# Optimization experiments

Measured on AMD Instinct MI355X. Metric: run time of the kernel, lower is better.

Reference implementation:

```python
import jax, jax.numpy as jnp
import numpy as np

B, N, F_IN, F_OUT, H = 2, 4096, 256, 64, 4


def setup_inputs() -> dict:
    key = jax.random.key(0)
    k_adj, k_h, k_w, k_l, k_r = jax.random.split(key, 5)
    adj = jax.random.randint(k_adj, (B, N, N), 0, 2, dtype=jnp.int32)
    h = jax.random.normal(k_h, (B, N, F_IN), dtype=jnp.float32)
    # xavier-uniform-ish params
    lim_w = float(np.sqrt(6.0 / (F_IN + F_OUT)))
    W = jax.random.uniform(k_w, (F_IN, F_OUT), jnp.float32, -lim_w, lim_w)
    lim_a = float(np.sqrt(6.0 / (F_OUT + H)))
    Wl = jax.random.uniform(k_l, (H, F_OUT), jnp.float32, -lim_a, lim_a)  # attn_l.weight
    Wr = jax.random.uniform(k_r, (H, F_OUT), jnp.float32, -lim_a, lim_a)  # attn_r.weight
    b = jnp.zeros((F_OUT,), jnp.float32)
    return {"adj": adj, "h": h, "W": W, "Wl": Wl, "Wr": Wr, "b": b}


def reference(adj, h, W, Wl, Wr, b):
    # dropout layers are identity in eval mode
    x = jnp.einsum('bnf,fo->bno', h, W)                       # (B,N,F_OUT)
    el = jnp.einsum('bno,ho->bnh', x, Wl)                     # (B,N,H)
    er = jnp.einsum('bno,ho->bnh', x, Wr)                     # (B,N,H)
    attn = el[:, :, None, :] + er[:, None, :, :]              # (B,N,N,H)
    attn = jax.nn.leaky_relu(attn, negative_slope=0.2)
    attn = jnp.where(adj[..., None] == 0, -jnp.inf, attn)
    attn = jax.nn.softmax(attn, axis=2)                       # softmax over source nodes j
    out = jnp.einsum('bijh,bjf->bihf', attn, x)               # (B,N,H,F_OUT)
    out = out + b                                             # bias over feature dim
    out = jax.nn.elu(out)                                     # activation
    return out.reshape(B, N, H * F_OUT)                       # n_heads>1 concat; B>1 keeps batch
```

## Files before the change

kernel.cpp:

```cpp
#include <hip/hip_runtime.h>
#include <hip/hip_bf16.h>


#define NN 4096
#define NH 4

typedef __bf16 bf16x8 __attribute__((ext_vector_type(8)));
typedef unsigned short ushortx8 __attribute__((ext_vector_type(8)));
typedef float f32x4 __attribute__((ext_vector_type(4)));

__device__ __forceinline__ void gload_lds16(const void* g, void* lds) {
  __builtin_amdgcn_global_load_lds(
      (const __attribute__((address_space(1))) void*)g,
      (__attribute__((address_space(3))) void*)lds, 16, 0, 0);
}

__device__ __forceinline__ unsigned short f2bf(float x) {
  __hip_bfloat16 hb = __float2bfloat16(x);
  return __builtin_bit_cast(unsigned short, hb);
}

__global__ __launch_bounds__(256) void gat_prep(
    const float* __restrict__ hmat, const float* __restrict__ W,
    const float* __restrict__ Wl, const float* __restrict__ Wr,
    unsigned short* __restrict__ xT, float* __restrict__ elT,
    float* __restrict__ erT)
{
  const int t = threadIdx.x;
  const int wv = t >> 6;
  const int l  = t & 63;
  const int b  = blockIdx.x >> 6;
  const int i0 = (blockIdx.x & 63) << 6;
  const int r0 = i0 + wv * 16;

  float wl[NH], wr[NH];
#pragma unroll
  for (int hh = 0; hh < NH; ++hh) { wl[hh] = Wl[hh*64 + l]; wr[hh] = Wr[hh*64 + l]; }

  float acc[16];
#pragma unroll
  for (int rr = 0; rr < 16; ++rr) acc[rr] = 0.f;

  const float* hbase = hmat + ((size_t)(b*NN + r0)) * 256;
  for (int k4 = 0; k4 < 64; ++k4) {
    float wv4[4];
#pragma unroll
    for (int kk = 0; kk < 4; ++kk) wv4[kk] = W[(k4*4 + kk)*64 + l];
#pragma unroll
    for (int rr = 0; rr < 16; ++rr) {
      const float4 hv = *(const float4*)(hbase + rr*256 + k4*4);
      acc[rr] = fmaf(hv.x, wv4[0], acc[rr]);
      acc[rr] = fmaf(hv.y, wv4[1], acc[rr]);
      acc[rr] = fmaf(hv.z, wv4[2], acc[rr]);
      acc[rr] = fmaf(hv.w, wv4[3], acc[rr]);
    }
  }

#pragma unroll
  for (int rr = 0; rr < 16; ++rr) {
    const int r = r0 + rr;
    xT[((size_t)(b*64 + l))*NN + r] = f2bf(acc[rr]);
#pragma unroll
    for (int hh = 0; hh < NH; ++hh) {
      float ev = acc[rr] * wl[hh];
      float rv = acc[rr] * wr[hh];
#pragma unroll
      for (int s = 1; s < 64; s <<= 1) {
        ev += __shfl_xor(ev, s, 64);
        rv += __shfl_xor(rv, s, 64);
      }
      if (l == 0) {
        elT[((size_t)b*NH + hh)*NN + r] = ev;
        erT[((size_t)b*NH + hh)*NN + r] = rv;
      }
    }
  }
}

__global__ __launch_bounds__(512, 2) void gat_main(
    const int* __restrict__ adj, const unsigned short* __restrict__ xT,
    const float* __restrict__ elT, const float* __restrict__ erT,
    const float* __restrict__ bias, float* __restrict__ out)
{
  __shared__ __align__(16) int            adj_lds[2][32*64];
  __shared__ __align__(16) unsigned short xt_lds[2][64*64];
  __shared__ __align__(16) float          er_lds[2][NH*64];
  __shared__ __align__(16) float          denom_lds[NH][32];

  const int t = threadIdx.x;
  const int w = t >> 6;
  const int l = t & 63;
  const int h = w >> 1;
  const int ihalf = w & 1;
  const int b  = blockIdx.x >> 7;
  const int i0 = (blockIdx.x & 127) << 5;

  const int lrow = l & 15;
  const int lk   = l >> 4;
  const int i_sc = (ihalf << 4) + lrow;
  const int swzi = (i_sc & 7) << 2;

  const float el_reg = elT[((size_t)b*NH + h)*NN + i0 + i_sc];

  auto issue_tile = [&](int j0, int bufi) {
    {
      const int ir = (w << 2) + (l >> 4);
      const int c  = (l & 15) ^ (ir & 7);
      gload_lds16(adj + ((size_t)(b*NN + i0 + ir))*NN + j0 + (c << 2),
                  &adj_lds[bufi][w*256]);
    }
    {
      const int fr_sub = l >> 3;
      const int c  = (l & 7) ^ fr_sub;
      gload_lds16(xT + ((size_t)(b*64 + (w<<3) + fr_sub))*NN + j0 + (c << 3),
                  &xt_lds[bufi][w*512]);
    }
    if (w == 0) {
      gload_lds16(erT + ((size_t)b*NH + (l >> 4))*NN + j0 + ((l & 15) << 2),
                  &er_lds[bufi][0]);
    }
  };

  f32x4 acc[4] = {};
  float dsum_acc = 0.f;

  issue_tile(0, 0);

  for (int it = 0; it < NN/64; ++it) {
    const int cur = it & 1;
    asm volatile("s_waitcnt vmcnt(0)" ::: "memory");
    __builtin_amdgcn_s_barrier();
    if (it + 1 < NN/64) issue_tile((it + 1) * 64, cur ^ 1);

    ushortx8 pa[2];
#pragma unroll
    for (int kc = 0; kc < 2; ++kc) {
      const int cbase = kc*32 + (lk << 3);
      const int4   aj0 = *(const int4*)  &adj_lds[cur][(i_sc*64 + cbase)     ^ swzi];
      const int4   aj1 = *(const int4*)  &adj_lds[cur][(i_sc*64 + cbase + 4) ^ swzi];
      const float4 er0 = *(const float4*)&er_lds[cur][h*64 + cbase];
      const float4 er1 = *(const float4*)&er_lds[cur][h*64 + cbase + 4];
#define SCORE(A, E, IDX) { \
        float s_ = el_reg + (E); \
        float lr_ = fmaxf(s_, 0.2f * s_); \
        float w_ = (A) ? __expf(lr_) : 0.0f; \
        dsum_acc += w_; \
        pa[kc][IDX] = f2bf(w_); }
      SCORE(aj0.x, er0.x, 0) SCORE(aj0.y, er0.y, 1)
      SCORE(aj0.z, er0.z, 2) SCORE(aj0.w, er0.w, 3)
      SCORE(aj1.x, er1.x, 4) SCORE(aj1.y, er1.y, 5)
      SCORE(aj1.z, er1.z, 6) SCORE(aj1.w, er1.w, 7)
#undef SCORE
    }

#pragma unroll
    for (int kc = 0; kc < 2; ++kc) {
      const bf16x8 A = __builtin_bit_cast(bf16x8, pa[kc]);
      const int jc = kc*32 + (lk << 3);
#pragma unroll
      for (int fq = 0; fq < 4; ++fq) {
        const int f = (fq << 4) + lrow;
        const int idx = (f*64 + jc) ^ ((f & 7) << 3);
        const bf16x8 B = __builtin_bit_cast(bf16x8, *(const ushortx8*)&xt_lds[cur][idx]);
        acc[fq] = __builtin_amdgcn_mfma_f32_16x16x32_bf16(A, B, acc[fq], 0, 0, 0);
      }
    }
  }

  float rs = dsum_acc;
  rs += __shfl_xor(rs, 16, 64);
  rs += __shfl_xor(rs, 32, 64);
  if (l < 16) denom_lds[h][(ihalf << 4) + l] = rs;
  __syncthreads();

  float inv[4];
#pragma unroll
  for (int r = 0; r < 4; ++r)
    inv[r] = 1.0f / denom_lds[h][(ihalf << 4) + (lk << 2) + r];

#pragma unroll
  for (int fq = 0; fq < 4; ++fq) {
    const int f = (fq << 4) + lrow;
    const float bv = bias[f];
#pragma unroll
    for (int r = 0; r < 4; ++r) {
      const int ir = (ihalf << 4) + (lk << 2) + r;
      float v = acc[fq][r] * inv[r] + bv;
      v = v > 0.f ? v : (__expf(v) - 1.f);
      out[(((size_t)b*NN + i0 + ir)*NH + h)*64 + f] = v;
    }
  }
}

extern "C" void kernel_launch(void* const* d_in, const int* in_sizes, int n_in,
                              void* d_out, int out_size, void* d_ws, size_t ws_size,
                              hipStream_t stream) {
  const int*   adj  = (const int*)d_in[0];
  const float* hmat = (const float*)d_in[1];
  const float* W    = (const float*)d_in[2];
  const float* Wl   = (const float*)d_in[3];
  const float* Wr   = (const float*)d_in[4];
  const float* bias = (const float*)d_in[5];
  float* out = (float*)d_out;

  unsigned short* xT = (unsigned short*)d_ws;
  float* elT = (float*)((char*)d_ws + (size_t)2*64*NN*2);
  float* erT = elT + (size_t)2*NH*NN;

  gat_prep<<<128, 256, 0, stream>>>(hmat, W, Wl, Wr, xT, elT, erT);
  gat_main<<<256, 512, 0, stream>>>(adj, xT, elT, erT, bias, out);
}
```

Baseline: 310.6 us.

## Retile GAT kernels: 16-row blocks, triple-buffered 128-wide tiles, MFMA row sums

The main kernel now handles 16 rows per 256-thread block, with one wave per head. It streams 128-column adjacency and feature tiles through a three-stage global-to-LDS pipeline with partial vmcnt waits. The softmax denominator is computed by an MFMA against a ones vector instead of scalar accumulation plus an LDS reduction. Exponentials use exp2 with log2e folded into el/er. The prep kernel is rewritten to stage h in LDS, use more blocks, and write transposed x with vector stores. Together these aim to hide adjacency load latency and raise parallelism, at the cost of more LDS per block and finely tuned wait counts that must match the number of issued loads.

```diff
diff --git a/kernel.cpp b/kernel.cpp
--- a/kernel.cpp
+++ b/kernel.cpp
@@ -4,9 +4,13 @@
 
 #define NN 4096
 #define NH 4
+#define JT 128
+#define NT (NN / JT)
+#define LOG2E 1.4426950408889634f
 
 typedef __bf16 bf16x8 __attribute__((ext_vector_type(8)));
 typedef unsigned short ushortx8 __attribute__((ext_vector_type(8)));
+typedef unsigned short us4 __attribute__((ext_vector_type(4)));
 typedef float f32x4 __attribute__((ext_vector_type(4)));
 
 __device__ __forceinline__ void gload_lds16(const void* g, void* lds) {
@@ -20,163 +24,182 @@
   return __builtin_bit_cast(unsigned short, hb);
 }
 
-__global__ __launch_bounds__(256) void gat_prep(
+#if __has_builtin(__builtin_amdgcn_exp2f)
+#define EXP2F(x) __builtin_amdgcn_exp2f(x)
+#else
+#define EXP2F(x) exp2f(x)
+#endif
+
+__global__ __launch_bounds__(256, 2) void gat_prep(
     const float* __restrict__ hmat, const float* __restrict__ W,
     const float* __restrict__ Wl, const float* __restrict__ Wr,
     unsigned short* __restrict__ xT, float* __restrict__ elT,
     float* __restrict__ erT)
 {
-  const int t = threadIdx.x;
+  __shared__ __align__(16) float h_s[16][256];
+  __shared__ float x_s[16][65];
+  __shared__ float wlr_s[512];
+
+  const int t  = threadIdx.x;
   const int wv = t >> 6;
   const int l  = t & 63;
-  const int b  = blockIdx.x >> 6;
-  const int i0 = (blockIdx.x & 63) << 6;
-  const int r0 = i0 + wv * 16;
-
-  float wl[NH], wr[NH];
-#pragma unroll
-  for (int hh = 0; hh < NH; ++hh) { wl[hh] = Wl[hh*64 + l]; wr[hh] = Wr[hh*64 + l]; }
-
-  float acc[16];
-#pragma unroll
-  for (int rr = 0; rr < 16; ++rr) acc[rr] = 0.f;
-
-  const float* hbase = hmat + ((size_t)(b*NN + r0)) * 256;
+  const int b  = blockIdx.x >> 8;
+  const int i0 = (blockIdx.x & 255) << 4;
+
+  {
+    const float4* hsrc = (const float4*)(hmat + ((size_t)(b * NN + i0)) * 256);
+    float4* hdst = (float4*)&h_s[0][0];
+#pragma unroll
+    for (int u = 0; u < 4; ++u) hdst[t + 256 * u] = hsrc[t + 256 * u];
+    wlr_s[t]       = Wl[t];
+    wlr_s[256 + t] = Wr[t];
+  }
+  __syncthreads();
+
+  const int row0 = wv << 2;
+  float acc[4] = {0.f, 0.f, 0.f, 0.f};
+#pragma unroll 4
   for (int k4 = 0; k4 < 64; ++k4) {
-    float wv4[4];
-#pragma unroll
-    for (int kk = 0; kk < 4; ++kk) wv4[kk] = W[(k4*4 + kk)*64 + l];
-#pragma unroll
-    for (int rr = 0; rr < 16; ++rr) {
-      const float4 hv = *(const float4*)(hbase + rr*256 + k4*4);
-      acc[rr] = fmaf(hv.x, wv4[0], acc[rr]);
-      acc[rr] = fmaf(hv.y, wv4[1], acc[rr]);
-      acc[rr] = fmaf(hv.z, wv4[2], acc[rr]);
-      acc[rr] = fmaf(hv.w, wv4[3], acc[rr]);
-    }
-  }
-
-#pragma unroll
-  for (int rr = 0; rr < 16; ++rr) {
-    const int r = r0 + rr;
-    xT[((size_t)(b*64 + l))*NN + r] = f2bf(acc[rr]);
-#pragma unroll
-    for (int hh = 0; hh < NH; ++hh) {
-      float ev = acc[rr] * wl[hh];
-      float rv = acc[rr] * wr[hh];
-#pragma unroll
-      for (int s = 1; s < 64; s <<= 1) {
-        ev += __shfl_xor(ev, s, 64);
-        rv += __shfl_xor(rv, s, 64);
-      }
-      if (l == 0) {
-        elT[((size_t)b*NH + hh)*NN + r] = ev;
-        erT[((size_t)b*NH + hh)*NN + r] = rv;
-      }
-    }
-  }
-}
-
-__global__ __launch_bounds__(512, 2) void gat_main(
+    const float w0 = W[(k4 * 4 + 0) * 64 + l];
+    const float w1 = W[(k4 * 4 + 1) * 64 + l];
+    const float w2 = W[(k4 * 4 + 2) * 64 + l];
+    const float w3 = W[(k4 * 4 + 3) * 64 + l];
+#pragma unroll
+    for (int rr = 0; rr < 4; ++rr) {
+      const float4 hv = *(const float4*)&h_s[row0 + rr][k4 * 4];
+      acc[rr] = fmaf(hv.x, w0, acc[rr]);
+      acc[rr] = fmaf(hv.y, w1, acc[rr]);
+      acc[rr] = fmaf(hv.z, w2, acc[rr]);
+      acc[rr] = fmaf(hv.w, w3, acc[rr]);
+    }
+  }
+#pragma unroll
+  for (int rr = 0; rr < 4; ++rr) x_s[row0 + rr][l] = acc[rr];
+  __syncthreads();
+
+  if (t < 64) {
+    const int row = t >> 2, hh = t & 3;
+    float el = 0.f, er = 0.f;
+#pragma unroll 8
+    for (int f = 0; f < 64; ++f) {
+      const float xv = x_s[row][f];
+      el = fmaf(xv, wlr_s[hh * 64 + f], el);
+      er = fmaf(xv, wlr_s[256 + hh * 64 + f], er);
+    }
+    elT[((size_t)b * NH + hh) * NN + i0 + row] = el * LOG2E;
+    erT[((size_t)b * NH + hh) * NN + i0 + row] = er * LOG2E;
+  }
+
+  {
+    const int f = t >> 2, q = t & 3;
+    us4 pk;
+#pragma unroll
+    for (int rj = 0; rj < 4; ++rj) pk[rj] = f2bf(x_s[q * 4 + rj][f]);
+    *(us4*)&xT[((size_t)(b * 64 + f)) * NN + i0 + q * 4] = pk;
+  }
+}
+
+__global__ __launch_bounds__(256, 2) void gat_main(
     const int* __restrict__ adj, const unsigned short* __restrict__ xT,
     const float* __restrict__ elT, const float* __restrict__ erT,
     const float* __restrict__ bias, float* __restrict__ out)
 {
-  __shared__ __align__(16) int            adj_lds[2][32*64];
-  __shared__ __align__(16) unsigned short xt_lds[2][64*64];
-  __shared__ __align__(16) float          er_lds[2][NH*64];
-  __shared__ __align__(16) float          denom_lds[NH][32];
+  __shared__ __align__(16) int            adj_lds[3][16 * JT];
+  __shared__ __align__(16) unsigned short xt_lds[3][64 * JT];
+  __shared__ __align__(16) float          er_lds[3][NH * JT];
 
   const int t = threadIdx.x;
   const int w = t >> 6;
   const int l = t & 63;
-  const int h = w >> 1;
-  const int ihalf = w & 1;
-  const int b  = blockIdx.x >> 7;
-  const int i0 = (blockIdx.x & 127) << 5;
+  const int b  = blockIdx.x >> 8;
+  const int i0 = (blockIdx.x & 255) << 4;
 
   const int lrow = l & 15;
   const int lk   = l >> 4;
-  const int i_sc = (ihalf << 4) + lrow;
-  const int swzi = (i_sc & 7) << 2;
-
-  const float el_reg = elT[((size_t)b*NH + h)*NN + i0 + i_sc];
-
-  auto issue_tile = [&](int j0, int bufi) {
-    {
-      const int ir = (w << 2) + (l >> 4);
-      const int c  = (l & 15) ^ (ir & 7);
-      gload_lds16(adj + ((size_t)(b*NN + i0 + ir))*NN + j0 + (c << 2),
-                  &adj_lds[bufi][w*256]);
-    }
-    {
-      const int fr_sub = l >> 3;
-      const int c  = (l & 7) ^ fr_sub;
-      gload_lds16(xT + ((size_t)(b*64 + (w<<3) + fr_sub))*NN + j0 + (c << 3),
-                  &xt_lds[bufi][w*512]);
-    }
-    if (w == 0) {
-      gload_lds16(erT + ((size_t)b*NH + (l >> 4))*NN + j0 + ((l & 15) << 2),
-                  &er_lds[bufi][0]);
+
+  const float el_reg = elT[((size_t)b * NH + w) * NN + i0 + lrow];
+
+  auto issue_tile = [&](int j0, int s) {
+#pragma unroll
+    for (int g = 0; g < 2; ++g) {
+      const int gi  = w * 2 + g;
+      const int row = gi * 2 + (l >> 5);
+      const int src = ((l & 31) ^ (row & 7)) << 2;
+      gload_lds16(adj + ((size_t)(b * NN + i0 + row)) * NN + j0 + src,
+                  &adj_lds[s][gi * 256]);
+    }
+#pragma unroll
+    for (int g = 0; g < 4; ++g) {
+      const int gi = w * 4 + g;
+      const int f  = gi * 4 + (l >> 4);
+      const int src = ((l & 15) ^ (f & 7)) << 3;
+      gload_lds16(xT + ((size_t)(b * 64 + f)) * NN + j0 + src,
+                  &xt_lds[s][gi * 512]);
+    }
+    if (w >= 2) {
+      const int h2 = (w - 2) * 2 + (l >> 5);
+      gload_lds16(erT + ((size_t)b * NH + h2) * NN + j0 + ((l & 31) << 2),
+                  &er_lds[s][(w - 2) * 256]);
     }
   };
 
   f32x4 acc[4] = {};
-  float dsum_acc = 0.f;
+  f32x4 accd = {};
+  ushortx8 ones_u;
+#pragma unroll
+  for (int i = 0; i < 8; ++i) ones_u[i] = 0x3F80;
+  const bf16x8 onesf = __builtin_bit_cast(bf16x8, ones_u);
 
   issue_tile(0, 0);
-
-  for (int it = 0; it < NN/64; ++it) {
-    const int cur = it & 1;
-    asm volatile("s_waitcnt vmcnt(0)" ::: "memory");
+  issue_tile(JT, 1);
+
+  for (int it = 0; it < NT; ++it) {
+    const int s = it % 3;
+    if (it == NT - 1)  asm volatile("s_waitcnt vmcnt(0)" ::: "memory");
+    else if (w < 2)    asm volatile("s_waitcnt vmcnt(6)" ::: "memory");
+    else               asm volatile("s_waitcnt vmcnt(7)" ::: "memory");
     __builtin_amdgcn_s_barrier();
-    if (it + 1 < NN/64) issue_tile((it + 1) * 64, cur ^ 1);
-
-    ushortx8 pa[2];
-#pragma unroll
-    for (int kc = 0; kc < 2; ++kc) {
-      const int cbase = kc*32 + (lk << 3);
-      const int4   aj0 = *(const int4*)  &adj_lds[cur][(i_sc*64 + cbase)     ^ swzi];
-      const int4   aj1 = *(const int4*)  &adj_lds[cur][(i_sc*64 + cbase + 4) ^ swzi];
-      const float4 er0 = *(const float4*)&er_lds[cur][h*64 + cbase];
-      const float4 er1 = *(const float4*)&er_lds[cur][h*64 + cbase + 4];
-#define SCORE(A, E, IDX) { \
-        float s_ = el_reg + (E); \
+    __builtin_amdgcn_sched_barrier(0);
+
+    if (it + 2 < NT) issue_tile((it + 2) * JT, (it + 2) % 3);
+
+#pragma unroll
+    for (int kc = 0; kc < 4; ++kc) {
+      const int cbase = kc * 32 + (lk << 3);
+      const int cq    = cbase >> 2;
+      const int4 aj0 = *(const int4*)&adj_lds[s][lrow * JT + ((cq ^ (lrow & 7)) << 2)];
+      const int4 aj1 = *(const int4*)&adj_lds[s][lrow * JT + (((cq + 1) ^ (lrow & 7)) << 2)];
+      const float4 er0 = *(const float4*)&er_lds[s][w * JT + cbase];
+      const float4 er1 = *(const float4*)&er_lds[s][w * JT + cbase + 4];
+
+      ushortx8 pa;
+#define SCORE(A_, E_, IDX) { \
+        float s_  = el_reg + (E_); \
         float lr_ = fmaxf(s_, 0.2f * s_); \
-        float w_ = (A) ? __expf(lr_) : 0.0f; \
-        dsum_acc += w_; \
-        pa[kc][IDX] = f2bf(w_); }
+        float w_  = (A_) ? EXP2F(lr_) : 0.0f; \
+        pa[IDX] = f2bf(w_); }
       SCORE(aj0.x, er0.x, 0) SCORE(aj0.y, er0.y, 1)
       SCORE(aj0.z, er0.z, 2) SCORE(aj0.w, er0.w, 3)
       SCORE(aj1.x, er1.x, 4) SCORE(aj1.y, er1.y, 5)
       SCORE(aj1.z, er1.z, 6) SCORE(aj1.w, er1.w, 7)
 #undef SCORE
-    }
-
-#pragma unroll
-    for (int kc = 0; kc < 2; ++kc) {
-      const bf16x8 A = __builtin_bit_cast(bf16x8, pa[kc]);
-      const int jc = kc*32 + (lk << 3);
+
+      const bf16x8 A = __builtin_bit_cast(bf16x8, pa);
+      accd = __builtin_amdgcn_mfma_f32_16x16x32_bf16(A, onesf, accd, 0, 0, 0);
 #pragma unroll
       for (int fq = 0; fq < 4; ++fq) {
-        const int f = (fq << 4) + lrow;
-        const int idx = (f*64 + jc) ^ ((f & 7) << 3);
-        const bf16x8 B = __builtin_bit_cast(bf16x8, *(const ushortx8*)&xt_lds[cur][idx]);
-        acc[fq] = __builtin_amdgcn_mfma_f32_16x16x32_bf16(A, B, acc[fq], 0, 0, 0);
+        const int f  = (fq << 4) + lrow;
+        const int cb = (kc << 2) + lk;
+        const int idx = f * JT + ((cb ^ (f & 7)) << 3);
+        const bf16x8 Bf = __builtin_bit_cast(bf16x8, *(const ushortx8*)&xt_lds[s][idx]);
+        acc[fq] = __builtin_amdgcn_mfma_f32_16x16x32_bf16(A, Bf, acc[fq], 0, 0, 0);
       }
     }
   }
 
-  float rs = dsum_acc;
-  rs += __shfl_xor(rs, 16, 64);
-  rs += __shfl_xor(rs, 32, 64);
-  if (l < 16) denom_lds[h][(ihalf << 4) + l] = rs;
-  __syncthreads();
-
   float inv[4];
 #pragma unroll
-  for (int r = 0; r < 4; ++r)
-    inv[r] = 1.0f / denom_lds[h][(ihalf << 4) + (lk << 2) + r];
+  for (int r = 0; r < 4; ++r) inv[r] = 1.0f / accd[r];
 
 #pragma unroll
   for (int fq = 0; fq < 4; ++fq) {
@@ -184,10 +207,10 @@
     const float bv = bias[f];
 #pragma unroll
     for (int r = 0; r < 4; ++r) {
-      const int ir = (ihalf << 4) + (lk << 2) + r;
+      const int ir = (lk << 2) + r;
       float v = acc[fq][r] * inv[r] + bv;
       v = v > 0.f ? v : (__expf(v) - 1.f);
-      out[(((size_t)b*NN + i0 + ir)*NH + h)*64 + f] = v;
+      out[(((size_t)b * NN + i0 + ir) * NH + w) * 64 + f] = v;
     }
   }
 }
@@ -204,9 +227,9 @@
   float* out = (float*)d_out;
 
   unsigned short* xT = (unsigned short*)d_ws;
-  float* elT = (float*)((char*)d_ws + (size_t)2*64*NN*2);
-  float* erT = elT + (size_t)2*NH*NN;
-
-  gat_prep<<<128, 256, 0, stream>>>(hmat, W, Wl, Wr, xT, elT, erT);
-  gat_main<<<256, 512, 0, stream>>>(adj, xT, elT, erT, bias, out);
-}
+  float* elT = (float*)((char*)d_ws + (size_t)2 * 64 * NN * 2);
+  float* erT = elT + (size_t)2 * NH * NN;
+
+  gat_prep<<<512, 256, 0, stream>>>(hmat, W, Wl, Wr, xT, elT, erT);
+  gat_main<<<512, 256, 0, stream>>>(adj, xT, elT, erT, bias, out);
+}
```

New measurement: 248.6 us. 20.0% less time.
